# Optimization experiments

Hardware: AMD Instinct MI355X
Metric: run time of the kernel (lower is better)

## Reference

```python
import jax, jax.numpy as jnp
import numpy as np
from jax import lax

HID = 512   # hidden_dim
DI = 1024   # d_inner = ssm_ratio * hidden_dim
N = 64      # ssm_d_state
R = 32      # dt_rank = ceil(512/16)
K = 4       # k_group
B, H, W = 4, 32, 32
MLP = 2048  # mlp_ratio * hidden_dim


def _ln(x, w, b):
    m = x.mean(-1, keepdims=True)
    v = ((x - m) ** 2).mean(-1, keepdims=True)
    return (x - m) / jnp.sqrt(v + 1e-5) * w + b


def setup_inputs() -> dict:
    key = jax.random.key(0)
    ks = jax.random.split(key, 12)
    rn = lambda k, s, sc: jax.random.normal(k, s, jnp.float32) * sc
    inp = {}
    inp["content"] = rn(ks[0], (B, H, W, HID), 1.0)
    inp["style"] = rn(ks[1], (B, H, W, HID), 1.0)
    inp["norm1_w"] = jnp.ones((HID,), jnp.float32)
    inp["norm1_b"] = jnp.zeros((HID,), jnp.float32)
    inp["in_proj_w"] = rn(ks[2], (HID, 2 * DI), HID ** -0.5)
    inp["conv_w"] = rn(ks[3], (DI, 1, 3, 3), 1.0 / 3.0)  # depthwise
    inp["conv_b"] = jnp.zeros((DI,), jnp.float32)
    inp["style_proj_w"] = rn(ks[4], (HID, K * (R + N)), HID ** -0.5)
    inp["content_proj_w"] = rn(ks[5], (DI, K * N), DI ** -0.5)
    inp["dt_projs_weight"] = rn(ks[6], (K, DI, R), R ** -0.5)
    inp["dt_projs_bias"] = rn(ks[7], (K, DI), 0.1)
    inp["A_logs"] = rn(ks[8], (K * DI, N), 0.1)
    inp["Ds"] = jnp.ones((K * DI,), jnp.float32)
    inp["out_proj_w"] = rn(ks[9], (DI, HID), DI ** -0.5)
    inp["norm2_w"] = jnp.ones((HID,), jnp.float32)
    inp["norm2_b"] = jnp.zeros((HID,), jnp.float32)
    inp["mlp_w1"] = rn(ks[10], (HID, MLP), HID ** -0.5)
    inp["mlp_b1"] = jnp.zeros((MLP,), jnp.float32)
    inp["mlp_w2"] = rn(ks[11], (MLP, HID), MLP ** -0.5)
    inp["mlp_b2"] = jnp.zeros((HID,), jnp.float32)
    return inp


def reference(content, style, norm1_w, norm1_b, in_proj_w, conv_w, conv_b,
              style_proj_w, content_proj_w, dt_projs_weight, dt_projs_bias,
              A_logs, Ds, out_proj_w, norm2_w, norm2_b,
              mlp_w1, mlp_b1, mlp_w2, mlp_b2):
    Bb, Hh, Ww, C = content.shape
    L = Hh * Ww
    res1 = content
    cn = _ln(content, norm1_w, norm1_b)
    sn = _ln(style, norm1_w, norm1_b)  # norm1 shared, as in source
    xz = cn @ in_proj_w                 # (B,H,W,2*DI)
    x, z = jnp.split(xz, 2, axis=-1)
    xc = x.transpose(0, 3, 1, 2)        # (B,DI,H,W)
    xconv = lax.conv_general_dilated(
        xc, conv_w, (1, 1), 'SAME', feature_group_count=DI,
        dimension_numbers=('NCHW', 'OIHW', 'NCHW')) + conv_b[None, :, None, None]
    xa = jax.nn.silu(xconv)             # (B,DI,H,W)
    # style-derived dt/B, content-derived C
    sp = (sn @ style_proj_w).reshape(Bb, L, K * (R + N))
    dts_rank, Bs = jnp.split(sp, [K * R], axis=-1)
    Cs = (xa.transpose(0, 2, 3, 1) @ content_proj_w).reshape(Bb, L, K * N)
    # cross_scan: 4 directions (raster, transposed raster, and their flips)
    xf = xa.reshape(Bb, DI, L)
    xt = xa.transpose(0, 1, 3, 2).reshape(Bb, DI, L)
    xs = jnp.stack([xf, xt, xf[..., ::-1], xt[..., ::-1]], axis=1)  # (B,K,DI,L)
    dts_rank = dts_rank.reshape(Bb, L, K, R).transpose(0, 2, 3, 1)   # (B,K,R,L)
    dts = jnp.einsum('bkrl,kdr->bkdl', dts_rank, dt_projs_weight)    # (B,K,DI,L)
    Bsm = Bs.reshape(Bb, L, K, N).transpose(0, 2, 3, 1)              # (B,K,N,L)
    Csm = Cs.reshape(Bb, L, K, N).transpose(0, 2, 3, 1)              # (B,K,N,L)
    A = -jnp.exp(A_logs.astype(jnp.float32)).reshape(K, DI, N)
    delta = jax.nn.softplus(dts + dt_projs_bias[None, :, :, None])   # (B,K,DI,L)
    # selective scan: h_t = exp(delta_t*A)*h_{t-1} + delta_t*B_t*u_t ; y_t = <h_t, C_t>
    def step(h, inpt):
        u_t, d_t, B_t, C_t = inpt  # (B,K,DI),(B,K,DI),(B,K,N),(B,K,N)
        h = jnp.exp(d_t[..., None] * A) * h + (d_t * u_t)[..., None] * B_t[:, :, None, :]
        y = jnp.einsum('bkdn,bkn->bkd', h, C_t)
        return h, y
    h0 = jnp.zeros((Bb, K, DI, N), jnp.float32)
    seq = (xs.transpose(3, 0, 1, 2), delta.transpose(3, 0, 1, 2),
           Bsm.transpose(3, 0, 1, 2), Csm.transpose(3, 0, 1, 2))
    _, ys = lax.scan(step, h0, seq)                                  # (L,B,K,DI)
    y_scan = ys.transpose(1, 2, 3, 0) + xs * Ds.reshape(K, DI)[None, :, :, None]
    # source sums the 4 directions without un-flipping (faithful)
    y = y_scan.reshape(Bb, K, DI, Hh, Ww).sum(1).transpose(0, 2, 3, 1)  # (B,H,W,DI)
    y = (y * z) @ out_proj_w
    x1 = res1 + y
    xn = _ln(x1, norm2_w, norm2_b)
    m = jax.nn.gelu(xn @ mlp_w1 + mlp_b1, approximate=False) @ mlp_w2 + mlp_b2
    return x1 + m
```

## Files before the change

### kernel.cpp

```cpp
#include <hip/hip_runtime.h>

#define B_ 4
#define Hh_ 32
#define Ww_ 32
#define L_ 1024
#define HID_ 512
#define DI_ 1024
#define N_ 64
#define R_ 32
#define K_ 4
#define MLP_ 2048

typedef __bf16 bf16x8 __attribute__((ext_vector_type(8)));
typedef float f32x4 __attribute__((ext_vector_type(4)));
typedef float v2f __attribute__((ext_vector_type(2)));

__device__ __forceinline__ unsigned short f2bf(float f) {
  unsigned int u = __builtin_bit_cast(unsigned int, f);
  return (unsigned short)((u + 0x7FFFu + ((u >> 16) & 1u)) >> 16);
}
__device__ __forceinline__ float bf2f(unsigned short h) {
  return __builtin_bit_cast(float, (unsigned int)h << 16);
}

template <int CTRL>
__device__ __forceinline__ float dpp_add(float x) {
  int i = __builtin_bit_cast(int, x);
  int j = __builtin_amdgcn_update_dpp(i, i, CTRL, 0xF, 0xF, false);
  return x + __builtin_bit_cast(float, j);
}

__global__ __launch_bounds__(256) void transpose_all(
    const float* __restrict__ s0, const float* __restrict__ s1,
    const float* __restrict__ s2, const float* __restrict__ s3,
    const float* __restrict__ s4, const float* __restrict__ s5,
    unsigned short* __restrict__ t0, unsigned short* __restrict__ t1,
    unsigned short* __restrict__ t2, unsigned short* __restrict__ t3,
    unsigned short* __restrict__ t4, unsigned short* __restrict__ t5) {
  __shared__ float t[32][33];
  int bid = blockIdx.x;
  const float* src; unsigned short* dst; int K, N, bx, by;
  if (bid < 1024)      { src = s0; dst = t0; K = 512;  N = 2048; int r = bid;        bx = r & 63; by = r >> 6; }
  else if (bid < 1216) { src = s1; dst = t1; K = 512;  N = 384;  int r = bid - 1024; bx = r % 12; by = r / 12; }
  else if (bid < 1472) { src = s2; dst = t2; K = 1024; N = 256;  int r = bid - 1216; bx = r & 7;  by = r >> 3; }
  else if (bid < 1984) { src = s3; dst = t3; K = 1024; N = 512;  int r = bid - 1472; bx = r & 15; by = r >> 4; }
  else if (bid < 3008) { src = s4; dst = t4; K = 512;  N = 2048; int r = bid - 1984; bx = r & 63; by = r >> 6; }
  else                 { src = s5; dst = t5; K = 2048; N = 512;  int r = bid - 3008; bx = r & 15; by = r >> 4; }
  int nb = bx * 32, kb = by * 32;
  int tx = threadIdx.x & 31, ty = threadIdx.x >> 5;
  for (int r = ty; r < 32; r += 8) t[r][tx] = src[(size_t)(kb + r) * N + nb + tx];
  __syncthreads();
  for (int r = ty; r < 32; r += 8) dst[(size_t)(nb + r) * K + kb + tx] = f2bf(t[tx][r]);
}

__global__ __launch_bounds__(256) void ln_kernel(
    const float* __restrict__ in0, unsigned short* __restrict__ out0,
    const float* __restrict__ in1, unsigned short* __restrict__ out1,
    const float* __restrict__ w, const float* __restrict__ bb) {
  const float* in = blockIdx.y ? in1 : in0;
  unsigned short* out = blockIdx.y ? out1 : out0;
  int row = blockIdx.x * 4 + (threadIdx.x >> 6);
  int lane = threadIdx.x & 63;
  const float* p = in + (size_t)row * HID_;
  float4 v0 = *(const float4*)(p + lane * 4);
  float4 v1 = *(const float4*)(p + 256 + lane * 4);
  float s = v0.x + v0.y + v0.z + v0.w + v1.x + v1.y + v1.z + v1.w;
  float q = v0.x * v0.x + v0.y * v0.y + v0.z * v0.z + v0.w * v0.w +
            v1.x * v1.x + v1.y * v1.y + v1.z * v1.z + v1.w * v1.w;
  #pragma unroll
  for (int m = 1; m < 64; m <<= 1) { s += __shfl_xor(s, m, 64); q += __shfl_xor(q, m, 64); }
  float mean = s * (1.f / 512.f);
  float var = q * (1.f / 512.f) - mean * mean;
  float rstd = rsqrtf(var + 1e-5f);
  float4 w0 = *(const float4*)(w + lane * 4);
  float4 w1 = *(const float4*)(w + 256 + lane * 4);
  float4 b0 = *(const float4*)(bb + lane * 4);
  float4 b1 = *(const float4*)(bb + 256 + lane * 4);
  unsigned short* o = out + (size_t)row * HID_;
  ushort4 r0, r1;
  r0.x = f2bf((v0.x - mean) * rstd * w0.x + b0.x);
  r0.y = f2bf((v0.y - mean) * rstd * w0.y + b0.y);
  r0.z = f2bf((v0.z - mean) * rstd * w0.z + b0.z);
  r0.w = f2bf((v0.w - mean) * rstd * w0.w + b0.w);
  r1.x = f2bf((v1.x - mean) * rstd * w1.x + b1.x);
  r1.y = f2bf((v1.y - mean) * rstd * w1.y + b1.y);
  r1.z = f2bf((v1.z - mean) * rstd * w1.z + b1.z);
  r1.w = f2bf((v1.w - mean) * rstd * w1.w + b1.w);
  *(ushort4*)(o + lane * 4) = r0;
  *(ushort4*)(o + 256 + lane * 4) = r1;
}

#define BM 128
#define BN 128
#define BK 64
#define LST 72

template <int EPI, int OUTBF>
__global__ __launch_bounds__(256) void gemm_kernel(
    const unsigned short* __restrict__ A, const unsigned short* __restrict__ BT,
    void* __restrict__ Cv, int M, int N, int K,
    const float* __restrict__ bias, const float* __restrict__ resid) {
  __shared__ __align__(16) unsigned short As[BM * LST];
  __shared__ __align__(16) unsigned short Bs[BN * LST];
  int tid = threadIdx.x;
  int lane = tid & 63, wv = tid >> 6;
  int wm = wv >> 1, wn = wv & 1;
  int nwg = gridDim.x * gridDim.y;
  int flat = blockIdx.y * gridDim.x + blockIdx.x;
  int swz = (flat & 7) * (nwg >> 3) + (flat >> 3);
  int bx = swz % gridDim.x, by = swz / gridDim.x;
  int m0 = by * BM, n0 = bx * BN;
  f32x4 acc[4][4] = {};
  int sr = tid >> 1, sc = (tid & 1) * 32;
  int rA = wm * 64 + (lane & 15);
  int rB = wn * 64 + (lane & 15);
  for (int k0 = 0; k0 < K; k0 += BK) {
    __syncthreads();
    {
      const unsigned short* Ap = A + (size_t)(m0 + sr) * K + k0 + sc;
      uint4 a0 = *(const uint4*)(Ap);
      uint4 a1 = *(const uint4*)(Ap + 8);
      uint4 a2 = *(const uint4*)(Ap + 16);
      uint4 a3 = *(const uint4*)(Ap + 24);
      unsigned short* Asp = &As[sr * LST + sc];
      *(uint4*)(Asp) = a0; *(uint4*)(Asp + 8) = a1;
      *(uint4*)(Asp + 16) = a2; *(uint4*)(Asp + 24) = a3;
      const unsigned short* Bp = BT + (size_t)(n0 + sr) * K + k0 + sc;
      uint4 b0 = *(const uint4*)(Bp);
      uint4 b1 = *(const uint4*)(Bp + 8);
      uint4 b2 = *(const uint4*)(Bp + 16);
      uint4 b3 = *(const uint4*)(Bp + 24);
      unsigned short* Bsp = &Bs[sr * LST + sc];
      *(uint4*)(Bsp) = b0; *(uint4*)(Bsp + 8) = b1;
      *(uint4*)(Bsp + 16) = b2; *(uint4*)(Bsp + 24) = b3;
    }
    __syncthreads();
    #pragma unroll
    for (int kx = 0; kx < 2; ++kx) {
      int kk = (lane >> 4) * 8 + kx * 32;
      bf16x8 fa[4], fb[4];
      #pragma unroll
      for (int i = 0; i < 4; ++i) {
        fa[i] = *(const bf16x8*)&As[(rA + i * 16) * LST + kk];
        fb[i] = *(const bf16x8*)&Bs[(rB + i * 16) * LST + kk];
      }
      #pragma unroll
      for (int i = 0; i < 4; ++i)
        #pragma unroll
        for (int j = 0; j < 4; ++j)
          acc[i][j] = __builtin_amdgcn_mfma_f32_16x16x32_bf16(fa[i], fb[j], acc[i][j], 0, 0, 0);
    }
  }
  int crow0 = m0 + wm * 64 + (lane >> 4) * 4, ccol0 = n0 + wn * 64 + (lane & 15);
  #pragma unroll
  for (int i = 0; i < 4; ++i) {
    #pragma unroll
    for (int j = 0; j < 4; ++j) {
      int col = ccol0 + j * 16;
      #pragma unroll
      for (int r = 0; r < 4; ++r) {
        int row = crow0 + i * 16 + r;
        float v = acc[i][j][r];
        if (EPI == 1) v += resid[(size_t)row * N + col];
        if (EPI == 2) { v += bias[col]; v = 0.5f * v * (1.f + erff(v * 0.70710678f)); }
        if (EPI == 3) v += bias[col] + resid[(size_t)row * N + col];
        if (OUTBF) ((unsigned short*)Cv)[(size_t)row * N + col] = f2bf(v);
        else       ((float*)Cv)[(size_t)row * N + col] = v;
      }
    }
  }
}

template <int EPI, int OUTBF>
__global__ __launch_bounds__(256) void gemm64_kernel(
    const unsigned short* __restrict__ A, const unsigned short* __restrict__ BT,
    void* __restrict__ Cv, int M, int N, int K,
    const float* __restrict__ bias, const float* __restrict__ resid) {
  __shared__ __align__(16) unsigned short As[64 * LST];
  __shared__ __align__(16) unsigned short Bs[128 * LST];
  int tid = threadIdx.x;
  int lane = tid & 63, wv = tid >> 6;
  int wm = wv >> 1, wn = wv & 1;
  int nwg = gridDim.x * gridDim.y;
  int flat = blockIdx.y * gridDim.x + blockIdx.x;
  int swz = (flat & 7) * (nwg >> 3) + (flat >> 3);
  int bx = swz % gridDim.x, by = swz / gridDim.x;
  int m0 = by * 64, n0 = bx * BN;
  f32x4 acc[2][4] = {};
  int srA = tid >> 2, scA = (tid & 3) * 16;
  int srB = tid >> 1, scB = (tid & 1) * 32;
  int rA = wm * 32 + (lane & 15);
  int rB = wn * 64 + (lane & 15);
  for (int k0 = 0; k0 < K; k0 += BK) {
    __syncthreads();
    {
      const unsigned short* Ap = A + (size_t)(m0 + srA) * K + k0 + scA;
      uint4 a0 = *(const uint4*)(Ap);
      uint4 a1 = *(const uint4*)(Ap + 8);
      unsigned short* Asp = &As[srA * LST + scA];
      *(uint4*)(Asp) = a0; *(uint4*)(Asp + 8) = a1;
      const unsigned short* Bp = BT + (size_t)(n0 + srB) * K + k0 + scB;
      uint4 b0 = *(const uint4*)(Bp);
      uint4 b1 = *(const uint4*)(Bp + 8);
      uint4 b2 = *(const uint4*)(Bp + 16);
      uint4 b3 = *(const uint4*)(Bp + 24);
      unsigned short* Bsp = &Bs[srB * LST + scB];
      *(uint4*)(Bsp) = b0; *(uint4*)(Bsp + 8) = b1;
      *(uint4*)(Bsp + 16) = b2; *(uint4*)(Bsp + 24) = b3;
    }
    __syncthreads();
    #pragma unroll
    for (int kx = 0; kx < 2; ++kx) {
      int kk = (lane >> 4) * 8 + kx * 32;
      bf16x8 fa[2], fb[4];
      #pragma unroll
      for (int i = 0; i < 2; ++i) fa[i] = *(const bf16x8*)&As[(rA + i * 16) * LST + kk];
      #pragma unroll
      for (int j = 0; j < 4; ++j) fb[j] = *(const bf16x8*)&Bs[(rB + j * 16) * LST + kk];
      #pragma unroll
      for (int i = 0; i < 2; ++i)
        #pragma unroll
        for (int j = 0; j < 4; ++j)
          acc[i][j] = __builtin_amdgcn_mfma_f32_16x16x32_bf16(fa[i], fb[j], acc[i][j], 0, 0, 0);
    }
  }
  int crow0 = m0 + wm * 32 + (lane >> 4) * 4, ccol0 = n0 + wn * 64 + (lane & 15);
  #pragma unroll
  for (int i = 0; i < 2; ++i) {
    #pragma unroll
    for (int j = 0; j < 4; ++j) {
      int col = ccol0 + j * 16;
      #pragma unroll
      for (int r = 0; r < 4; ++r) {
        int row = crow0 + i * 16 + r;
        float v = acc[i][j][r];
        if (EPI == 1) v += resid[(size_t)row * N + col];
        if (EPI == 2) { v += bias[col]; v = 0.5f * v * (1.f + erff(v * 0.70710678f)); }
        if (EPI == 3) v += bias[col] + resid[(size_t)row * N + col];
        if (OUTBF) ((unsigned short*)Cv)[(size_t)row * N + col] = f2bf(v);
        else       ((float*)Cv)[(size_t)row * N + col] = v;
      }
    }
  }
}

__global__ __launch_bounds__(256) void conv_kernel(
    const unsigned short* __restrict__ xz, const float* __restrict__ cw,
    const float* __restrict__ cb, unsigned short* __restrict__ xa) {
  int idx = blockIdx.x * 256 + threadIdx.x;
  int d = idx & (DI_ - 1);
  int l = (idx >> 10) & (L_ - 1);
  int b = idx >> 20;
  int hh = l >> 5, ww = l & 31;
  float acc = cb[d];
  #pragma unroll
  for (int dh = -1; dh <= 1; ++dh) {
    int y = hh + dh;
    if ((unsigned)y >= 32u) continue;
    #pragma unroll
    for (int dw = -1; dw <= 1; ++dw) {
      int x = ww + dw;
      if ((unsigned)x >= 32u) continue;
      acc = fmaf(bf2f(xz[((size_t)b * L_ + y * 32 + x) * (2 * DI_) + d]),
                 cw[d * 9 + (dh + 1) * 3 + (dw + 1)], acc);
    }
  }
  float sv = acc / (1.f + __expf(-acc));
  xa[idx] = f2bf(sv);
}

__global__ __launch_bounds__(256) void delta_kernel(
    const float* __restrict__ sp, const float* __restrict__ dtw,
    const float* __restrict__ dtb, unsigned short* __restrict__ delta) {
  int bk = blockIdx.x;
  int b = bk >> 2, k = bk & 3;
  int dc = blockIdx.y * 256;
  int l0 = blockIdx.z * 128;
  __shared__ float wl[32 * 257];
  __shared__ float rl[128 * 32];
  int tid = threadIdx.x;
  for (int i = tid; i < 256 * 32; i += 256) {
    int dl = i >> 5, r = i & 31;
    wl[r * 257 + dl] = dtw[((size_t)k * DI_ + dc + dl) * R_ + r];
  }
  for (int i = tid; i < 128 * 32; i += 256) {
    int ll = i >> 5, r = i & 31;
    rl[ll * 32 + r] = sp[((size_t)b * L_ + l0 + ll) * 384 + k * R_ + r];
  }
  __syncthreads();
  float bias = dtb[k * DI_ + dc + tid];
  for (int ll = 0; ll < 128; ++ll) {
    float acc = bias;
    #pragma unroll
    for (int r = 0; r < 32; ++r)
      acc = fmaf(rl[ll * 32 + r], wl[r * 257 + tid], acc);
    float dlt = (acc > 15.f) ? acc : log1pf(__expf(acc));
    delta[(((size_t)(b * 4 + k) * L_) + l0 + ll) * DI_ + dc + tid] = f2bf(dlt);
  }
}

#define CH 16
#define NCH (L_ / CH)
#define DLP 36
#define YQP 6
__global__ __launch_bounds__(512) void scan_kernel(
    unsigned short* __restrict__ ybuf, const unsigned short* __restrict__ xa,
    const float* __restrict__ sp, const float* __restrict__ Cs,
    const unsigned short* __restrict__ dltb,
    const float* __restrict__ A_logs, const float* __restrict__ Ds) {
  int dblk = blockIdx.x;
  int k = blockIdx.y, b = blockIdx.z;
  int tid = threadIdx.x, lane = tid & 63, wv = tid >> 6;
  int dg = lane >> 4, ng = lane & 15;
  int qp = (lane >> 2) & 3;
  int wd = wv * 4 + dg;
  int gd = k * DI_ + dblk * 32 + wd;
  v2f a2p[2], h2[2];
  #pragma unroll
  for (int j = 0; j < 2; ++j) {
    a2p[j].x = -__expf(A_logs[(size_t)gd * N_ + ng * 4 + 2 * j]) * 1.44269504f;
    a2p[j].y = -__expf(A_logs[(size_t)gd * N_ + ng * 4 + 2 * j + 1]) * 1.44269504f;
    h2[j].x = 0.f; h2[j].y = 0.f;
  }

  __shared__ float Bsh[2][CH][64];
  __shared__ float Csh[2][CH][64];
  __shared__ float DLU[2][32][DLP];
  __shared__ float yq[CH][32][YQP];
  __shared__ float dsh[32];

  const size_t spB = (size_t)b * L_ * 384 + 128 + k * 64;
  const size_t csB = (size_t)b * L_ * 256 + k * 64;
  const size_t dlB = ((size_t)(b * 4 + k) * L_) * DI_ + dblk * 32;
  const size_t xaB = (size_t)b * L_ * DI_ + dblk * 32;

  if (tid < 32) dsh[tid] = Ds[k * DI_ + dblk * 32 + tid];

  int liS = tid >> 5, js = tid & 31;
  int liE = tid >> 5, dd = tid & 31;
  auto posf = [&](int l) {
    int lr = 1023 - l;
    return (k == 0) ? l
         : (k == 1) ? ((l & 31) * 32 + (l >> 5))
         : (k == 2) ? lr
                    : ((lr & 31) * 32 + (lr >> 5));
  };

  {
    *(float2*)&Bsh[0][liS][js * 2] = *(const float2*)(sp + spB + (size_t)liS * 384 + js * 2);
    *(float2*)&Csh[0][liS][js * 2] = *(const float2*)(Cs + csB + (size_t)liS * 256 + js * 2);
    float2 p;
    p.x = bf2f(dltb[dlB + (size_t)liS * DI_ + js]);
    p.y = bf2f(xa[xaB + (size_t)posf(liS) * DI_ + js]);
    *(float2*)&DLU[0][js][liS * 2] = p;
  }
  __syncthreads();

  int cur = 0;
  for (int c = 0; c < NCH; ++c) {
    float2 pB, pC;
    unsigned short pD, pU;
    if (c < NCH - 1) {
      int lb = (c + 1) * CH + liS;
      pB = *(const float2*)(sp + spB + (size_t)lb * 384 + js * 2);
      pC = *(const float2*)(Cs + csB + (size_t)lb * 256 + js * 2);
      pD = dltb[dlB + (size_t)lb * DI_ + js];
      pU = xa[xaB + (size_t)posf(lb) * DI_ + js];
    }
    #pragma unroll
    for (int li2 = 0; li2 < CH; li2 += 2) {
      f32x4 duq = *(const f32x4*)&DLU[cur][wd][li2 * 2];
      #pragma unroll
      for (int s = 0; s < 2; ++s) {
        int li = li2 + s;
        float dlt = s ? duq[2] : duq[0];
        float u   = s ? duq[3] : duq[1];
        float du = dlt * u;
        f32x4 bq = *(const f32x4*)&Bsh[cur][li][ng * 4];
        f32x4 cq = *(const f32x4*)&Csh[cur][li][ng * 4];
        v2f b01 = __builtin_shufflevector(bq, bq, 0, 1);
        v2f b23 = __builtin_shufflevector(bq, bq, 2, 3);
        v2f c01 = __builtin_shufflevector(cq, cq, 0, 1);
        v2f c23 = __builtin_shufflevector(cq, cq, 2, 3);
        v2f dlt2; dlt2.x = dlt; dlt2.y = dlt;
        v2f du2;  du2.x = du;  du2.y = du;
        v2f arg0 = dlt2 * a2p[0];
        v2f arg1 = dlt2 * a2p[1];
        v2f e0, e1;
        e0.x = __builtin_amdgcn_exp2f(arg0.x);
        e0.y = __builtin_amdgcn_exp2f(arg0.y);
        e1.x = __builtin_amdgcn_exp2f(arg1.x);
        e1.y = __builtin_amdgcn_exp2f(arg1.y);
        h2[0] = e0 * h2[0] + du2 * b01;
        h2[1] = e1 * h2[1] + du2 * b23;
        v2f yv = h2[0] * c01 + h2[1] * c23;
        float yp = yv.x + yv.y;
        yp = dpp_add<0xB1>(yp);
        yp = dpp_add<0x4E>(yp);
        yq[li][wd][qp] = yp;
      }
    }
    __syncthreads();
    {
      float2 q01 = *(const float2*)&yq[liE][dd][0];
      float2 q23 = *(const float2*)&yq[liE][dd][2];
      float y = (q01.x + q01.y) + (q23.x + q23.y);
      float u = DLU[cur][dd][liE * 2 + 1];
      y = fmaf(u, dsh[dd], y);
      ybuf[dlB + (size_t)(c * CH + liE) * DI_ + dd] = f2bf(y);
    }
    if (c < NCH - 1) {
      int nxt = cur ^ 1;
      *(float2*)&Bsh[nxt][liS][js * 2] = pB;
      *(float2*)&Csh[nxt][liS][js * 2] = pC;
      float2 p; p.x = bf2f(pD); p.y = bf2f(pU);
      *(float2*)&DLU[nxt][js][liS * 2] = p;
    }
    __syncthreads();
    cur ^= 1;
  }
}

__global__ __launch_bounds__(256) void fuse_ygz(
    const unsigned short* __restrict__ yk, const unsigned short* __restrict__ xz,
    unsigned short* __restrict__ ygz) {
  size_t i = ((size_t)blockIdx.x * 256 + threadIdx.x) * 8;
  size_t b = i >> 20, ld = i & ((1u << 20) - 1);
  float acc[8] = {};
  #pragma unroll
  for (int k = 0; k < 4; ++k) {
    uint4 v = *(const uint4*)(yk + ((size_t)(b * 4 + k) << 20) + ld);
    unsigned int w[4] = {v.x, v.y, v.z, v.w};
    #pragma unroll
    for (int t = 0; t < 4; ++t) {
      acc[t * 2 + 0] += __builtin_bit_cast(float, w[t] << 16);
      acc[t * 2 + 1] += __builtin_bit_cast(float, w[t] & 0xFFFF0000u);
    }
  }
  uint4 zv = *(const uint4*)(xz + (i >> 10) * (2 * DI_) + DI_ + (i & (DI_ - 1)));
  unsigned int zw[4] = {zv.x, zv.y, zv.z, zv.w};
  float z[8];
  #pragma unroll
  for (int t = 0; t < 4; ++t) {
    z[t * 2 + 0] = __builtin_bit_cast(float, zw[t] << 16);
    z[t * 2 + 1] = __builtin_bit_cast(float, zw[t] & 0xFFFF0000u);
  }
  uint4 o;
  o.x = (unsigned int)f2bf(acc[0] * z[0]) | ((unsigned int)f2bf(acc[1] * z[1]) << 16);
  o.y = (unsigned int)f2bf(acc[2] * z[2]) | ((unsigned int)f2bf(acc[3] * z[3]) << 16);
  o.z = (unsigned int)f2bf(acc[4] * z[4]) | ((unsigned int)f2bf(acc[5] * z[5]) << 16);
  o.w = (unsigned int)f2bf(acc[6] * z[6]) | ((unsigned int)f2bf(acc[7] * z[7]) << 16);
  *(uint4*)(ygz + i) = o;
}

extern "C" void kernel_launch(void* const* d_in, const int* in_sizes, int n_in,
                              void* d_out, int out_size, void* d_ws, size_t ws_size,
                              hipStream_t stream) {
  (void)in_sizes; (void)n_in; (void)out_size; (void)ws_size;
  const float* content   = (const float*)d_in[0];
  const float* style     = (const float*)d_in[1];
  const float* norm1_w   = (const float*)d_in[2];
  const float* norm1_b   = (const float*)d_in[3];
  const float* in_proj_w = (const float*)d_in[4];
  const float* conv_w    = (const float*)d_in[5];
  const float* conv_b    = (const float*)d_in[6];
  const float* style_proj_w   = (const float*)d_in[7];
  const float* content_proj_w = (const float*)d_in[8];
  const float* dtw       = (const float*)d_in[9];
  const float* dtb       = (const float*)d_in[10];
  const float* A_logs    = (const float*)d_in[11];
  const float* Ds        = (const float*)d_in[12];
  const float* out_proj_w = (const float*)d_in[13];
  const float* norm2_w   = (const float*)d_in[14];
  const float* norm2_b   = (const float*)d_in[15];
  const float* mlp_w1    = (const float*)d_in[16];
  const float* mlp_b1    = (const float*)d_in[17];
  const float* mlp_w2    = (const float*)d_in[18];
  const float* mlp_b2    = (const float*)d_in[19];
  float* out = (float*)d_out;

  float* ws = (float*)d_ws;
  const size_t ROWS = (size_t)B_ * L_;
  const size_t SCAN_ELEMS = (size_t)B_ * K_ * L_ * DI_;
  size_t o = 0;
  unsigned short* cn  = (unsigned short*)(ws + o); o += ROWS * HID_ / 2;
  unsigned short* sn  = (unsigned short*)(ws + o); o += ROWS * HID_ / 2;
  unsigned short* xn  = (unsigned short*)(ws + o); o += ROWS * HID_ / 2;
  unsigned short* xz  = (unsigned short*)(ws + o); o += ROWS * 2 * DI_ / 2;
  float* sp    = ws + o; o += ROWS * 384;
  unsigned short* xa = (unsigned short*)(ws + o); o += ROWS * DI_ / 2;
  float* csb   = ws + o; o += ROWS * 256;
  float* x1    = ws + o; o += ROWS * HID_;
  unsigned short* dltb = (unsigned short*)(ws + o); o += SCAN_ELEMS / 2;
  unsigned short* ybuf = (unsigned short*)(ws + o); o += SCAN_ELEMS / 2;
  unsigned short* ygz  = (unsigned short*)(ws + o); o += ROWS * DI_ / 2;
  unsigned short* wt = (unsigned short*)(ws + o);
  unsigned short* inpT = wt;
  unsigned short* styT = inpT + 2048 * 512;
  unsigned short* conT = styT + 384 * 512;
  unsigned short* outT = conT + 256 * 1024;
  unsigned short* w1T  = outT + 512 * 1024;
  unsigned short* w2T  = w1T + 2048 * 512;
  unsigned short* hmid = ybuf;

  transpose_all<<<4032, 256, 0, stream>>>(
      in_proj_w, style_proj_w, content_proj_w, out_proj_w, mlp_w1, mlp_w2,
      inpT, styT, conT, outT, w1T, w2T);

  ln_kernel<<<dim3(ROWS / 4, 2), 256, 0, stream>>>(content, cn, style, sn, norm1_w, norm1_b);

  gemm_kernel<0, 1><<<dim3(2048 / BN, ROWS / BM), 256, 0, stream>>>(
      cn, inpT, xz, ROWS, 2048, 512, nullptr, nullptr);
  gemm64_kernel<0, 0><<<dim3(384 / BN, ROWS / 64), 256, 0, stream>>>(
      sn, styT, sp, ROWS, 384, 512, nullptr, nullptr);
  conv_kernel<<<(ROWS * DI_) / 256, 256, 0, stream>>>(xz, conv_w, conv_b, xa);
  gemm64_kernel<0, 0><<<dim3(256 / BN, ROWS / 64), 256, 0, stream>>>(
      xa, conT, csb, ROWS, 256, 1024, nullptr, nullptr);
  delta_kernel<<<dim3(B_ * K_, DI_ / 256, L_ / 128), 256, 0, stream>>>(sp, dtw, dtb, dltb);
  scan_kernel<<<dim3(DI_ / 32, K_, B_), 512, 0, stream>>>(
      ybuf, xa, sp, csb, dltb, A_logs, Ds);
  fuse_ygz<<<(ROWS * DI_) / (256 * 8), 256, 0, stream>>>(ybuf, xz, ygz);
  gemm64_kernel<1, 0><<<dim3(512 / BN, ROWS / 64), 256, 0, stream>>>(
      ygz, outT, x1, ROWS, 512, 1024, nullptr, content);
  ln_kernel<<<dim3(ROWS / 4, 1), 256, 0, stream>>>(x1, xn, nullptr, nullptr, norm2_w, norm2_b);
  gemm_kernel<2, 1><<<dim3(2048 / BN, ROWS / BM), 256, 0, stream>>>(
      xn, w1T, hmid, ROWS, 2048, 512, mlp_b1, nullptr);
  gemm64_kernel<3, 0><<<dim3(512 / BN, ROWS / 64), 256, 0, stream>>>(
      hmid, w2T, out, ROWS, 512, 2048, mlp_b2, x1);
}
```

Before: 493.7 us.

## Load GEMM tiles directly to LDS with XOR-swizzled layout

Both GEMM kernels now use global_load_lds (direct global-to-LDS DMA, 16 bytes per lane) instead of loading into registers and then storing to shared memory. The padded LDS stride is replaced by an unpadded 64-wide tile with an XOR swizzle of 16-byte blocks, which avoids bank conflicts and saves LDS space. This removes the staging VGPRs and the ds_write instructions, but keeps the single-buffered, fully synchronised loop. It depends on the swizzle matching between the writer lanes and the fragment reads.

```diff
diff --git a/kernel.cpp b/kernel.cpp
--- a/kernel.cpp
+++ b/kernel.cpp
@@ -21,6 +21,12 @@
 }
 __device__ __forceinline__ float bf2f(unsigned short h) {
   return __builtin_bit_cast(float, (unsigned int)h << 16);
+}
+
+__device__ __forceinline__ void gload16(const unsigned short* g, unsigned short* l) {
+  __builtin_amdgcn_global_load_lds(
+      (const __attribute__((address_space(1))) unsigned int*)g,
+      (__attribute__((address_space(3))) unsigned int*)l, 16, 0, 0);
 }
 
 template <int CTRL>
@@ -93,15 +99,14 @@
 #define BM 128
 #define BN 128
 #define BK 64
-#define LST 72
 
 template <int EPI, int OUTBF>
 __global__ __launch_bounds__(256) void gemm_kernel(
     const unsigned short* __restrict__ A, const unsigned short* __restrict__ BT,
     void* __restrict__ Cv, int M, int N, int K,
     const float* __restrict__ bias, const float* __restrict__ resid) {
-  __shared__ __align__(16) unsigned short As[BM * LST];
-  __shared__ __align__(16) unsigned short Bs[BN * LST];
+  __shared__ __align__(16) unsigned short As[BM * BK];
+  __shared__ __align__(16) unsigned short Bs[BN * BK];
   int tid = threadIdx.x;
   int lane = tid & 63, wv = tid >> 6;
   int wm = wv >> 1, wn = wv & 1;
@@ -111,38 +116,29 @@
   int bx = swz % gridDim.x, by = swz / gridDim.x;
   int m0 = by * BM, n0 = bx * BN;
   f32x4 acc[4][4] = {};
-  int sr = tid >> 1, sc = (tid & 1) * 32;
+  int rowblk = lane >> 3;
+  int sblk = (lane & 7) ^ rowblk;
   int rA = wm * 64 + (lane & 15);
   int rB = wn * 64 + (lane & 15);
   for (int k0 = 0; k0 < K; k0 += BK) {
     __syncthreads();
-    {
-      const unsigned short* Ap = A + (size_t)(m0 + sr) * K + k0 + sc;
-      uint4 a0 = *(const uint4*)(Ap);
-      uint4 a1 = *(const uint4*)(Ap + 8);
-      uint4 a2 = *(const uint4*)(Ap + 16);
-      uint4 a3 = *(const uint4*)(Ap + 24);
-      unsigned short* Asp = &As[sr * LST + sc];
-      *(uint4*)(Asp) = a0; *(uint4*)(Asp + 8) = a1;
-      *(uint4*)(Asp + 16) = a2; *(uint4*)(Asp + 24) = a3;
-      const unsigned short* Bp = BT + (size_t)(n0 + sr) * K + k0 + sc;
-      uint4 b0 = *(const uint4*)(Bp);
-      uint4 b1 = *(const uint4*)(Bp + 8);
-      uint4 b2 = *(const uint4*)(Bp + 16);
-      uint4 b3 = *(const uint4*)(Bp + 24);
-      unsigned short* Bsp = &Bs[sr * LST + sc];
-      *(uint4*)(Bsp) = b0; *(uint4*)(Bsp + 8) = b1;
-      *(uint4*)(Bsp + 16) = b2; *(uint4*)(Bsp + 24) = b3;
+    #pragma unroll
+    for (int it = 0; it < 4; ++it) {
+      int r0 = wv * 32 + it * 8;
+      gload16(A + (size_t)(m0 + r0 + rowblk) * K + k0 + sblk * 8, &As[r0 * BK]);
+      gload16(BT + (size_t)(n0 + r0 + rowblk) * K + k0 + sblk * 8, &Bs[r0 * BK]);
     }
     __syncthreads();
     #pragma unroll
     for (int kx = 0; kx < 2; ++kx) {
-      int kk = (lane >> 4) * 8 + kx * 32;
+      int bidx = (lane >> 4) + kx * 4;
       bf16x8 fa[4], fb[4];
       #pragma unroll
       for (int i = 0; i < 4; ++i) {
-        fa[i] = *(const bf16x8*)&As[(rA + i * 16) * LST + kk];
-        fb[i] = *(const bf16x8*)&Bs[(rB + i * 16) * LST + kk];
+        int ra = rA + i * 16;
+        int rb = rB + i * 16;
+        fa[i] = *(const bf16x8*)&As[ra * BK + ((bidx ^ (ra & 7)) << 3)];
+        fb[i] = *(const bf16x8*)&Bs[rb * BK + ((bidx ^ (rb & 7)) << 3)];
       }
       #pragma unroll
       for (int i = 0; i < 4; ++i)
@@ -176,8 +172,8 @@
     const unsigned short* __restrict__ A, const unsigned short* __restrict__ BT,
     void* __restrict__ Cv, int M, int N, int K,
     const float* __restrict__ bias, const float* __restrict__ resid) {
-  __shared__ __align__(16) unsigned short As[64 * LST];
-  __shared__ __align__(16) unsigned short Bs[128 * LST];
+  __shared__ __align__(16) unsigned short As[64 * BK];
+  __shared__ __align__(16) unsigned short Bs[128 * BK];
   int tid = threadIdx.x;
   int lane = tid & 63, wv = tid >> 6;
   int wm = wv >> 1, wn = wv & 1;
@@ -187,36 +183,37 @@
   int bx = swz % gridDim.x, by = swz / gridDim.x;
   int m0 = by * 64, n0 = bx * BN;
   f32x4 acc[2][4] = {};
-  int srA = tid >> 2, scA = (tid & 3) * 16;
-  int srB = tid >> 1, scB = (tid & 1) * 32;
+  int rowblk = lane >> 3;
+  int sblk = (lane & 7) ^ rowblk;
   int rA = wm * 32 + (lane & 15);
   int rB = wn * 64 + (lane & 15);
   for (int k0 = 0; k0 < K; k0 += BK) {
     __syncthreads();
-    {
-      const unsigned short* Ap = A + (size_t)(m0 + srA) * K + k0 + scA;
-      uint4 a0 = *(const uint4*)(Ap);
-      uint4 a1 = *(const uint4*)(Ap + 8);
-      unsigned short* Asp = &As[srA * LST + scA];
-      *(uint4*)(Asp) = a0; *(uint4*)(Asp + 8) = a1;
-      const unsigned short* Bp = BT + (size_t)(n0 + srB) * K + k0 + scB;
-      uint4 b0 = *(const uint4*)(Bp);
-      uint4 b1 = *(const uint4*)(Bp + 8);
-      uint4 b2 = *(const uint4*)(Bp + 16);
-      uint4 b3 = *(const uint4*)(Bp + 24);
-      unsigned short* Bsp = &Bs[srB * LST + scB];
-      *(uint4*)(Bsp) = b0; *(uint4*)(Bsp + 8) = b1;
-      *(uint4*)(Bsp + 16) = b2; *(uint4*)(Bsp + 24) = b3;
+    #pragma unroll
+    for (int it = 0; it < 2; ++it) {
+      int r0 = wv * 16 + it * 8;
+      gload16(A + (size_t)(m0 + r0 + rowblk) * K + k0 + sblk * 8, &As[r0 * BK]);
+    }
+    #pragma unroll
+    for (int it = 0; it < 4; ++it) {
+      int r0 = wv * 32 + it * 8;
+      gload16(BT + (size_t)(n0 + r0 + rowblk) * K + k0 + sblk * 8, &Bs[r0 * BK]);
     }
     __syncthreads();
     #pragma unroll
     for (int kx = 0; kx < 2; ++kx) {
-      int kk = (lane >> 4) * 8 + kx * 32;
+      int bidx = (lane >> 4) + kx * 4;
       bf16x8 fa[2], fb[4];
       #pragma unroll
-      for (int i = 0; i < 2; ++i) fa[i] = *(const bf16x8*)&As[(rA + i * 16) * LST + kk];
-      #pragma unroll
-      for (int j = 0; j < 4; ++j) fb[j] = *(const bf16x8*)&Bs[(rB + j * 16) * LST + kk];
+      for (int i = 0; i < 2; ++i) {
+        int ra = rA + i * 16;
+        fa[i] = *(const bf16x8*)&As[ra * BK + ((bidx ^ (ra & 7)) << 3)];
+      }
+      #pragma unroll
+      for (int j = 0; j < 4; ++j) {
+        int rb = rB + j * 16;
+        fb[j] = *(const bf16x8*)&Bs[rb * BK + ((bidx ^ (rb & 7)) << 3)];
+      }
       #pragma unroll
       for (int i = 0; i < 2; ++i)
         #pragma unroll
```

Measured after the change: 464.0 us. 1.06x faster.
